# Kernel optimization log

Measured on AMD Instinct MI355X. Metric: run time of the kernel, lower is better.

The kernel has to match this reference:

```python
import jax, jax.numpy as jnp
import numpy as np
from jax import lax

B, T = 64, 2048
RNN_DIM, EMB_DIM, ATT_DIM = 1024, 512, 128
N_FILT, KSIZE = 32, 31
PAD = (KSIZE - 1) // 2


def setup_inputs() -> dict:
    key = jax.random.key(0)
    ks = jax.random.split(key, 9)
    return {
        "query": jax.random.normal(ks[0], (B, RNN_DIM), jnp.float32),
        "processed_memory": jax.random.normal(ks[1], (B, T, ATT_DIM), jnp.float32),
        "attention_weights_cat": jax.random.uniform(ks[2], (B, 2, T), jnp.float32),
        "mask": jax.random.randint(ks[3], (B, T), 0, 2).astype(bool),
        "memory": jax.random.normal(ks[4], (B, T, EMB_DIM), jnp.float32),
        # learned parameters (torch Linear stores weight as [out, in])
        "W_query": jax.random.normal(ks[5], (ATT_DIM, RNN_DIM), jnp.float32) * 0.05,
        "conv_w": jax.random.normal(ks[6], (N_FILT, 2, KSIZE), jnp.float32) * 0.05,
        "W_loc": jax.random.normal(ks[7], (ATT_DIM, N_FILT), jnp.float32) * 0.05,
        "v_w": jax.random.normal(ks[8], (1, ATT_DIM), jnp.float32) * 0.05,
    }


def reference(query, processed_memory, attention_weights_cat, mask, memory,
              W_query, conv_w, W_loc, v_w):
    # processed_query: [B, 1, A]
    processed_query = (query @ W_query.T)[:, None, :]
    # location features: conv over time (2 -> N_FILT channels), same padding
    loc = lax.conv_general_dilated(
        attention_weights_cat, conv_w, window_strides=(1,),
        padding=[(PAD, PAD)], dimension_numbers=("NCH", "OIH", "NCH"))  # [B, F, T]
    processed_loc = jnp.einsum("bft,af->bta", loc, W_loc)  # [B, T, A]
    # additive energies -> [B, T]
    energies = jnp.tanh(processed_loc + processed_memory + processed_query) @ v_w[0]
    energies = jnp.where(mask, -jnp.inf, energies)
    attention_weights = jax.nn.softmax(energies, axis=1)  # [B, T]
    attention_context = jnp.einsum("bt,btd->bd", attention_weights, memory)  # [B, D]
    return attention_context, attention_weights
```

## Files before the change

kernel.cpp:

```cpp
#include <hip/hip_runtime.h>
#include <math.h>

#define B_ 64
#define T_ 2048
#define RNN_DIM 1024
#define EMB_DIM 512
#define ATT_DIM 128
#define N_FILT 32
#define KSIZE 31
#define PAD_ 15
#define TT 64
#define NSLICE 32
#define NPART 64

__device__ __forceinline__ float fast_tanh(float x) {
    float e = __expf(2.0f * x);
    return 1.0f - 2.0f / (e + 1.0f);
}

__global__ __launch_bounds__(256) void k_pq(const float* __restrict__ query,
                                            const float* __restrict__ Wq,
                                            float* __restrict__ pq) {
    __shared__ float4 q4s[RNN_DIM / 4];
    __shared__ float red[4][64];
    const int b = blockIdx.y;
    const int tid = threadIdx.x;
    q4s[tid] = reinterpret_cast<const float4*>(query + (size_t)b * RNN_DIM)[tid];
    __syncthreads();
    const int al = tid & 63;
    const int rp = tid >> 6;
    const int a  = blockIdx.x * 64 + al;
    const float4* w4 = reinterpret_cast<const float4*>(Wq + (size_t)a * RNN_DIM) + rp * 64;
    float acc = 0.f;
    #pragma unroll 8
    for (int i = 0; i < 64; ++i) {
        float4 w = w4[i];
        float4 q = q4s[rp * 64 + i];
        acc += w.x * q.x + w.y * q.y + w.z * q.z + w.w * q.w;
    }
    red[rp][al] = acc;
    __syncthreads();
    if (tid < 64) {
        float r = red[0][tid] + red[1][tid] + red[2][tid] + red[3][tid];
        pq[b * ATT_DIM + blockIdx.x * 64 + tid] = r;
    }
}

__global__ __launch_bounds__(256) void k_fused(
    const float* __restrict__ att,
    const float* __restrict__ pm,
    const float* __restrict__ cw,
    const float* __restrict__ Wl,
    const float* __restrict__ v,
    const float* __restrict__ pq,
    const int*   __restrict__ mask,
    const float* __restrict__ mem,
    float* __restrict__ P,
    float* __restrict__ part)
{
    __shared__ float att_s[2][TT + KSIZE - 1];
    __shared__ float loc_s[N_FILT][TT];
    __shared__ float pm_s[TT * (ATT_DIM + 1)];
    __shared__ float ep_s[4][TT];
    __shared__ float p_s[TT];
    __shared__ int   msk_s[TT];

    const int b   = blockIdx.y;
    const int ts  = blockIdx.x;
    const int t0  = ts * TT;
    const int tid = threadIdx.x;
    const int lane = tid & 63;
    const int w    = __builtin_amdgcn_readfirstlane(tid >> 6);

    if (tid < TT) msk_s[tid] = mask[b * T_ + t0 + tid];
    if (tid < 2 * (TT + KSIZE - 1)) {
        int c = tid / (TT + KSIZE - 1);
        int i = tid % (TT + KSIZE - 1);
        int gt = t0 + i - PAD_;
        att_s[c][i] = (gt >= 0 && gt < T_) ? att[(b * 2 + c) * T_ + gt] : 0.f;
    }
    __syncthreads();

    {
        const float4* src4 = reinterpret_cast<const float4*>(
            pm + ((size_t)b * T_ + t0) * ATT_DIM);
        #pragma unroll
        for (int j = 0; j < TT * ATT_DIM / 4 / 256; ++j) {
            int idx = tid + 256 * j;
            int row = idx >> 5;
            if (msk_s[row] == 0) {
                int c4  = idx & 31;
                float4 vv = src4[idx];
                float* dst = pm_s + row * (ATT_DIM + 1) + c4 * 4;
                dst[0] = vv.x; dst[1] = vv.y; dst[2] = vv.z; dst[3] = vv.w;
            }
        }
    }
    __syncthreads();

    #pragma unroll
    for (int p = 0; p < 2; ++p) {
        int fb = __builtin_amdgcn_readfirstlane(w * 8 + p * 4);
        float a0 = 0.f, a1 = 0.f, a2 = 0.f, a3 = 0.f;
        #pragma unroll
        for (int c = 0; c < 2; ++c) {
            #pragma unroll
            for (int k = 0; k < KSIZE; ++k) {
                float av = att_s[c][lane + k];
                a0 += av * cw[((fb + 0) * 2 + c) * KSIZE + k];
                a1 += av * cw[((fb + 1) * 2 + c) * KSIZE + k];
                a2 += av * cw[((fb + 2) * 2 + c) * KSIZE + k];
                a3 += av * cw[((fb + 3) * 2 + c) * KSIZE + k];
            }
        }
        loc_s[fb + 0][lane] = a0;
        loc_s[fb + 1][lane] = a1;
        loc_s[fb + 2][lane] = a2;
        loc_s[fb + 3][lane] = a3;
    }
    __syncthreads();

    float lreg[N_FILT];
    #pragma unroll
    for (int f = 0; f < N_FILT; ++f) lreg[f] = loc_s[f][lane];

    const float* pm_row = pm_s + lane * (ATT_DIM + 1);
    const float* pq_row = pq + b * ATT_DIM;
    float eacc = 0.f;
    const int abase = __builtin_amdgcn_readfirstlane(w * 32);
    #pragma unroll 2
    for (int j = 0; j < 32; ++j) {
        int a = abase + j;
        const float* wl_row = Wl + a * N_FILT;
        float pl = 0.f;
        #pragma unroll
        for (int f = 0; f < N_FILT; ++f)
            pl += wl_row[f] * lreg[f];
        float x = pl + pm_row[a] + pq_row[a];
        eacc += fast_tanh(x) * v[a];
    }
    ep_s[w][lane] = eacc;
    __syncthreads();

    if (tid < TT) {
        float e = ep_s[0][tid] + ep_s[1][tid] + ep_s[2][tid] + ep_s[3][tid];
        float p = (msk_s[tid] != 0) ? 0.f : __expf(e);
        P[b * T_ + t0 + tid] = p;
        p_s[tid] = p;
    }
    __syncthreads();

    const int g  = tid >> 7;
    const int d4 = tid & 127;
    const float4* m4 = reinterpret_cast<const float4*>(mem)
                     + ((size_t)b * T_ + t0 + g * 32) * (EMB_DIM / 4);
    float4 acc = make_float4(0.f, 0.f, 0.f, 0.f);
    #pragma unroll 4
    for (int i = 0; i < 32; ++i) {
        float wt = p_s[g * 32 + i];
        if (wt != 0.f) {
            float4 mv = m4[(size_t)i * (EMB_DIM / 4) + d4];
            acc.x += wt * mv.x; acc.y += wt * mv.y;
            acc.z += wt * mv.z; acc.w += wt * mv.w;
        }
    }
    reinterpret_cast<float4*>(part)[
        ((size_t)(b * NPART + ts * 2 + g)) * (EMB_DIM / 4) + d4] = acc;
}

__global__ __launch_bounds__(256) void k_combine(
    const float* __restrict__ part,
    float* __restrict__ W,
    float* __restrict__ ctx)
{
    __shared__ float red[4];
    const int b = blockIdx.x, tid = threadIdx.x;
    float p[T_ / 256];
    float s = 0.f;
    #pragma unroll
    for (int j = 0; j < T_ / 256; ++j) {
        p[j] = W[b * T_ + tid + 256 * j];
        s += p[j];
    }
    #pragma unroll
    for (int off = 32; off >= 1; off >>= 1)
        s += __shfl_xor(s, off, 64);
    if ((tid & 63) == 0) red[tid >> 6] = s;
    __syncthreads();
    const float S = red[0] + red[1] + red[2] + red[3];
    const float inv = 1.0f / S;
    #pragma unroll
    for (int j = 0; j < T_ / 256; ++j)
        W[b * T_ + tid + 256 * j] = p[j] * inv;
    #pragma unroll
    for (int j = 0; j < EMB_DIM / 256; ++j) {
        int d = tid + 256 * j;
        float acc = 0.f;
        #pragma unroll
        for (int sl = 0; sl < NPART; ++sl)
            acc += part[((size_t)b * NPART + sl) * EMB_DIM + d];
        ctx[b * EMB_DIM + d] = acc * inv;
    }
}

extern "C" void kernel_launch(void* const* d_in, const int* in_sizes, int n_in,
                              void* d_out, int out_size, void* d_ws, size_t ws_size,
                              hipStream_t stream) {
    const float* query = (const float*)d_in[0];
    const float* pm    = (const float*)d_in[1];
    const float* att   = (const float*)d_in[2];
    const int*   mask  = (const int*)d_in[3];
    const float* mem   = (const float*)d_in[4];
    const float* Wq    = (const float*)d_in[5];
    const float* cw    = (const float*)d_in[6];
    const float* Wl    = (const float*)d_in[7];
    const float* vw    = (const float*)d_in[8];

    float* ctx = (float*)d_out;
    float* wts = (float*)d_out + B_ * EMB_DIM;
    float* pq   = (float*)d_ws;
    float* part = pq + B_ * ATT_DIM;

    k_pq     <<<dim3(2, B_),        dim3(256), 0, stream>>>(query, Wq, pq);
    k_fused  <<<dim3(NSLICE, B_),   dim3(256), 0, stream>>>(att, pm, cw, Wl, vw, pq, mask, mem, wts, part);
    k_combine<<<dim3(B_),           dim3(256), 0, stream>>>(part, wts, ctx);
}
```

Before: 437.7 us.

## Fuse combine kernel into main kernel via last-block atomic counter reduction

```diff
diff --git a/kernel.cpp b/kernel.cpp
--- a/kernel.cpp
+++ b/kernel.cpp
@@ -11,7 +11,6 @@
 #define PAD_ 15
 #define TT 64
 #define NSLICE 32
-#define NPART 64
 
 __device__ __forceinline__ float fast_tanh(float x) {
     float e = __expf(2.0f * x);
@@ -20,11 +19,13 @@
 
 __global__ __launch_bounds__(256) void k_pq(const float* __restrict__ query,
                                             const float* __restrict__ Wq,
-                                            float* __restrict__ pq) {
+                                            float* __restrict__ pq,
+                                            int* __restrict__ cnt) {
     __shared__ float4 q4s[RNN_DIM / 4];
     __shared__ float red[4][64];
     const int b = blockIdx.y;
     const int tid = threadIdx.x;
+    if (blockIdx.x == 0 && blockIdx.y == 0 && tid < B_) cnt[tid] = 0;
     q4s[tid] = reinterpret_cast<const float4*>(query + (size_t)b * RNN_DIM)[tid];
     __syncthreads();
     const int al = tid & 63;
@@ -56,7 +57,9 @@
     const int*   __restrict__ mask,
     const float* __restrict__ mem,
     float* __restrict__ P,
-    float* __restrict__ part)
+    float* __restrict__ part,
+    int*   __restrict__ cnt,
+    float* __restrict__ ctx)
 {
     __shared__ float att_s[2][TT + KSIZE - 1];
     __shared__ float loc_s[N_FILT][TT];
@@ -64,6 +67,8 @@
     __shared__ float ep_s[4][TT];
     __shared__ float p_s[TT];
     __shared__ int   msk_s[TT];
+    __shared__ float4 half_s[EMB_DIM / 4];
+    __shared__ int   last_s;
 
     const int b   = blockIdx.y;
     const int ts  = blockIdx.x;
@@ -164,42 +169,49 @@
             acc.z += wt * mv.z; acc.w += wt * mv.w;
         }
     }
-    reinterpret_cast<float4*>(part)[
-        ((size_t)(b * NPART + ts * 2 + g)) * (EMB_DIM / 4) + d4] = acc;
-}
-
-__global__ __launch_bounds__(256) void k_combine(
-    const float* __restrict__ part,
-    float* __restrict__ W,
-    float* __restrict__ ctx)
-{
-    __shared__ float red[4];
-    const int b = blockIdx.x, tid = threadIdx.x;
-    float p[T_ / 256];
+    if (g == 1) half_s[d4] = acc;
+    __syncthreads();
+    if (g == 0) {
+        float4 hv = half_s[d4];
+        acc.x += hv.x; acc.y += hv.y; acc.z += hv.z; acc.w += hv.w;
+        reinterpret_cast<float4*>(part)[
+            ((size_t)(b * NSLICE + ts)) * (EMB_DIM / 4) + d4] = acc;
+    }
+
+    __threadfence();
+    if (tid == 0) {
+        int done = atomicAdd(&cnt[b], 1);
+        last_s = (done == NSLICE - 1);
+    }
+    __syncthreads();
+    if (!last_s) return;
+    __threadfence();
+
+    float pv[T_ / 256];
     float s = 0.f;
     #pragma unroll
     for (int j = 0; j < T_ / 256; ++j) {
-        p[j] = W[b * T_ + tid + 256 * j];
-        s += p[j];
+        pv[j] = P[b * T_ + tid + 256 * j];
+        s += pv[j];
     }
     #pragma unroll
     for (int off = 32; off >= 1; off >>= 1)
         s += __shfl_xor(s, off, 64);
-    if ((tid & 63) == 0) red[tid >> 6] = s;
-    __syncthreads();
-    const float S = red[0] + red[1] + red[2] + red[3];
+    if ((tid & 63) == 0) ep_s[0][tid >> 6] = s;
+    __syncthreads();
+    const float S = ep_s[0][0] + ep_s[0][1] + ep_s[0][2] + ep_s[0][3];
     const float inv = 1.0f / S;
     #pragma unroll
     for (int j = 0; j < T_ / 256; ++j)
-        W[b * T_ + tid + 256 * j] = p[j] * inv;
+        P[b * T_ + tid + 256 * j] = pv[j] * inv;
     #pragma unroll
     for (int j = 0; j < EMB_DIM / 256; ++j) {
         int d = tid + 256 * j;
-        float acc = 0.f;
-        #pragma unroll
-        for (int sl = 0; sl < NPART; ++sl)
-            acc += part[((size_t)b * NPART + sl) * EMB_DIM + d];
-        ctx[b * EMB_DIM + d] = acc * inv;
+        float accd = 0.f;
+        #pragma unroll
+        for (int sl = 0; sl < NSLICE; ++sl)
+            accd += part[((size_t)b * NSLICE + sl) * EMB_DIM + d];
+        ctx[b * EMB_DIM + d] = accd * inv;
     }
 }
 
@@ -220,8 +232,9 @@
     float* wts = (float*)d_out + B_ * EMB_DIM;
     float* pq   = (float*)d_ws;
     float* part = pq + B_ * ATT_DIM;
-
-    k_pq     <<<dim3(2, B_),        dim3(256), 0, stream>>>(query, Wq, pq);
-    k_fused  <<<dim3(NSLICE, B_),   dim3(256), 0, stream>>>(att, pm, cw, Wl, vw, pq, mask, mem, wts, part);
-    k_combine<<<dim3(B_),           dim3(256), 0, stream>>>(part, wts, ctx);
-}
+    int*   cnt  = (int*)(part + (size_t)B_ * NSLICE * EMB_DIM);
+
+    k_pq    <<<dim3(2, B_),      dim3(256), 0, stream>>>(query, Wq, pq, cnt);
+    k_fused <<<dim3(NSLICE, B_), dim3(256), 0, stream>>>(att, pm, cw, Wl, vw, pq,
+                                                         mask, mem, wts, part, cnt, ctx);
+}
```

Measured after the change: 775.5 us. 77.2% more time.

## Load processed_memory into registers and reduce partials in-block

Applied to the files above, without the earlier changes.

```diff
diff --git a/kernel.cpp b/kernel.cpp
--- a/kernel.cpp
+++ b/kernel.cpp
@@ -11,7 +11,6 @@
 #define PAD_ 15
 #define TT 64
 #define NSLICE 32
-#define NPART 64
 
 __device__ __forceinline__ float fast_tanh(float x) {
     float e = __expf(2.0f * x);
@@ -46,7 +45,7 @@
     }
 }
 
-__global__ __launch_bounds__(256) void k_fused(
+__global__ __launch_bounds__(256, 4) void k_fused(
     const float* __restrict__ att,
     const float* __restrict__ pm,
     const float* __restrict__ cw,
@@ -60,10 +59,9 @@
 {
     __shared__ float att_s[2][TT + KSIZE - 1];
     __shared__ float loc_s[N_FILT][TT];
-    __shared__ float pm_s[TT * (ATT_DIM + 1)];
     __shared__ float ep_s[4][TT];
     __shared__ float p_s[TT];
-    __shared__ int   msk_s[TT];
+    __shared__ float4 half_s[EMB_DIM / 4];
 
     const int b   = blockIdx.y;
     const int ts  = blockIdx.x;
@@ -72,29 +70,28 @@
     const int lane = tid & 63;
     const int w    = __builtin_amdgcn_readfirstlane(tid >> 6);
 
-    if (tid < TT) msk_s[tid] = mask[b * T_ + t0 + tid];
+    const int mym = mask[b * T_ + t0 + lane];
+
+    float pmv[32];
+    if (mym == 0) {
+        const float4* prow = reinterpret_cast<const float4*>(
+            pm + ((size_t)b * T_ + t0 + lane) * ATT_DIM) + w * 8;
+        #pragma unroll
+        for (int i = 0; i < 8; ++i) {
+            float4 t4 = prow[i];
+            pmv[4 * i + 0] = t4.x; pmv[4 * i + 1] = t4.y;
+            pmv[4 * i + 2] = t4.z; pmv[4 * i + 3] = t4.w;
+        }
+    } else {
+        #pragma unroll
+        for (int i = 0; i < 32; ++i) pmv[i] = 0.f;
+    }
+
     if (tid < 2 * (TT + KSIZE - 1)) {
         int c = tid / (TT + KSIZE - 1);
         int i = tid % (TT + KSIZE - 1);
         int gt = t0 + i - PAD_;
         att_s[c][i] = (gt >= 0 && gt < T_) ? att[(b * 2 + c) * T_ + gt] : 0.f;
-    }
-    __syncthreads();
-
-    {
-        const float4* src4 = reinterpret_cast<const float4*>(
-            pm + ((size_t)b * T_ + t0) * ATT_DIM);
-        #pragma unroll
-        for (int j = 0; j < TT * ATT_DIM / 4 / 256; ++j) {
-            int idx = tid + 256 * j;
-            int row = idx >> 5;
-            if (msk_s[row] == 0) {
-                int c4  = idx & 31;
-                float4 vv = src4[idx];
-                float* dst = pm_s + row * (ATT_DIM + 1) + c4 * 4;
-                dst[0] = vv.x; dst[1] = vv.y; dst[2] = vv.z; dst[3] = vv.w;
-            }
-        }
     }
     __syncthreads();
 
@@ -124,11 +121,10 @@
     #pragma unroll
     for (int f = 0; f < N_FILT; ++f) lreg[f] = loc_s[f][lane];
 
-    const float* pm_row = pm_s + lane * (ATT_DIM + 1);
     const float* pq_row = pq + b * ATT_DIM;
     float eacc = 0.f;
     const int abase = __builtin_amdgcn_readfirstlane(w * 32);
-    #pragma unroll 2
+    #pragma unroll
     for (int j = 0; j < 32; ++j) {
         int a = abase + j;
         const float* wl_row = Wl + a * N_FILT;
@@ -136,7 +132,7 @@
         #pragma unroll
         for (int f = 0; f < N_FILT; ++f)
             pl += wl_row[f] * lreg[f];
-        float x = pl + pm_row[a] + pq_row[a];
+        float x = pl + pmv[j] + pq_row[a];
         eacc += fast_tanh(x) * v[a];
     }
     ep_s[w][lane] = eacc;
@@ -144,7 +140,7 @@
 
     if (tid < TT) {
         float e = ep_s[0][tid] + ep_s[1][tid] + ep_s[2][tid] + ep_s[3][tid];
-        float p = (msk_s[tid] != 0) ? 0.f : __expf(e);
+        float p = (mym != 0) ? 0.f : __expf(e);
         P[b * T_ + t0 + tid] = p;
         p_s[tid] = p;
     }
@@ -164,8 +160,14 @@
             acc.z += wt * mv.z; acc.w += wt * mv.w;
         }
     }
-    reinterpret_cast<float4*>(part)[
-        ((size_t)(b * NPART + ts * 2 + g)) * (EMB_DIM / 4) + d4] = acc;
+    if (g == 1) half_s[d4] = acc;
+    __syncthreads();
+    if (g == 0) {
+        float4 hv = half_s[d4];
+        acc.x += hv.x; acc.y += hv.y; acc.z += hv.z; acc.w += hv.w;
+        reinterpret_cast<float4*>(part)[
+            ((size_t)(b * NSLICE + ts)) * (EMB_DIM / 4) + d4] = acc;
+    }
 }
 
 __global__ __launch_bounds__(256) void k_combine(
@@ -197,8 +199,8 @@
         int d = tid + 256 * j;
         float acc = 0.f;
         #pragma unroll
-        for (int sl = 0; sl < NPART; ++sl)
-            acc += part[((size_t)b * NPART + sl) * EMB_DIM + d];
+        for (int sl = 0; sl < NSLICE; ++sl)
+            acc += part[((size_t)b * NSLICE + sl) * EMB_DIM + d];
         ctx[b * EMB_DIM + d] = acc * inv;
     }
 }
@@ -221,7 +223,8 @@
     float* pq   = (float*)d_ws;
     float* part = pq + B_ * ATT_DIM;
 
-    k_pq     <<<dim3(2, B_),        dim3(256), 0, stream>>>(query, Wq, pq);
-    k_fused  <<<dim3(NSLICE, B_),   dim3(256), 0, stream>>>(att, pm, cw, Wl, vw, pq, mask, mem, wts, part);
-    k_combine<<<dim3(B_),           dim3(256), 0, stream>>>(part, wts, ctx);
-}
+    k_pq     <<<dim3(2, B_),      dim3(256), 0, stream>>>(query, Wq, pq);
+    k_fused  <<<dim3(NSLICE, B_), dim3(256), 0, stream>>>(att, pm, cw, Wl, vw, pq,
+                                                          mask, mem, wts, part);
+    k_combine<<<dim3(B_),         dim3(256), 0, stream>>>(part, wts, ctx);
+}
```

After: 442.9 us. About the same (+1.2%).
